# Kernel optimization log

Measured on AMD Instinct MI355X. Metric: run time of the kernel, lower is better.

Reference implementation:

```python
import jax, jax.numpy as jnp
import numpy as np

B, D, O = 128, 1024, 512
EPS = 1e-5

def setup_inputs() -> dict:
    key = jax.random.key(0)
    ks = jax.random.split(key, 12)
    s = 0.02  # truncated-normal-ish scale
    glorot1 = float(np.sqrt(6.0 / (D + O)))
    glorot3 = float(np.sqrt(6.0 / (3 * O + O)))
    return {
        "x": jax.random.normal(ks[0], (B, D), jnp.float32),
        "gt": jax.random.normal(ks[1], (D, O), jnp.float32) * s,
        "wt": jax.random.normal(ks[2], (D, O), jnp.float32) * s,
        "mt": jax.random.normal(ks[3], (D, O), jnp.float32) * s,
        "kernel_1": jax.random.uniform(ks[4], (D, O), jnp.float32, -glorot1, glorot1),
        "bias_1": jnp.zeros((O,), jnp.float32),
        "kernel_3": jax.random.uniform(ks[5], (3 * O, O), jnp.float32, -glorot3, glorot3),
        "bias_3": jnp.zeros((O,), jnp.float32),
        "emb_kernel": jax.random.normal(ks[6], (1, 1, 3 * O), jnp.float32) * s,  # conv1d kernel [1, in=1, 3O]
        "emb_bias": jnp.zeros((3 * O,), jnp.float32),
        "embeding_k": jax.random.normal(ks[7], (1, D, 1), jnp.float32) * s,
        "norm_g": jnp.ones((O,), jnp.float32),
        "norm_b": jnp.zeros((O,), jnp.float32),
    }

def reference(x, gt, wt, mt, kernel_1, bias_1, kernel_3, bias_3,
              emb_kernel, emb_bias, embeding_k, norm_g, norm_b):
    # perceptron cell (identity activation)
    c1 = x @ kernel_1 + bias_1                                  # [B,O]
    # NALU cell
    wa = jnp.tanh(wt) * jax.nn.sigmoid(mt)                      # [D,O]
    g = jax.nn.sigmoid(x @ gt)                                  # [B,O]
    a = x @ wa                                                  # [B,O]
    m = jnp.sinh(jnp.arcsinh(x) @ wa)                           # [B,O]
    c3 = g * a + (1.0 - g) * m                                  # [B,O]
    # test cell: per-feature self-attention
    e = x[..., None] * emb_kernel.reshape(1, 1, -1) + emb_bias  # [B,D,3O]
    q, k, v = jnp.split(e, 3, axis=-1)                          # each [B,D,O]
    scale = jax.lax.rsqrt(jnp.asarray(v.shape[-1], x.dtype))
    w = jnp.einsum('bdo,beo->bde', q, k) * scale                # [B,D,D]
    w = jax.nn.softmax(w, axis=-1)
    att = jnp.einsum('bde,beo->bdo', w, v)                      # [B,D,O]
    s = jnp.sum(att * embeding_k, axis=1)                       # [B,O]
    u = jnp.mean(s, axis=-1, keepdims=True)
    var = jnp.mean(jnp.square(s - u), axis=-1, keepdims=True)
    c4 = (s - u) * jax.lax.rsqrt(var + EPS) * norm_g + norm_b   # [B,O]
    feat = jnp.concatenate([c1, c3, c4], axis=-1)               # [B,3O]
    return feat @ kernel_3 + bias_3                             # [B,O]
```

## Files before the change

### kernel.cpp

```cpp
#include <hip/hip_runtime.h>
#include <hip/hip_bf16.h>
#include <math.h>

typedef unsigned short u16;
typedef unsigned int u32;
typedef __attribute__((ext_vector_type(8))) short bf16x8;
typedef __attribute__((ext_vector_type(4))) float f32x4;

#define NB 128
#define ND 1024
#define NO 512
#define EPSV 1e-5f
#define SCALEQK 0.04419417382415922f
#define LOG2E 1.4426950408889634f

static __device__ __forceinline__ float fast_exp2(float v) {
#if __has_builtin(__builtin_amdgcn_exp2f)
  return __builtin_amdgcn_exp2f(v);
#else
  return exp2f(v);
#endif
}
static __device__ __forceinline__ float fast_rcp(float v) {
#if __has_builtin(__builtin_amdgcn_rcpf)
  return __builtin_amdgcn_rcpf(v);
#else
  return 1.f / v;
#endif
}
static __device__ __forceinline__ u16 bf16_rtn(float f) {
  unsigned u = __float_as_uint(f);
  return (u16)((u + 0x7FFFu + ((u >> 16) & 1u)) >> 16);
}
static __device__ __forceinline__ float asinh_fast(float x) {
  const float ax = fabsf(x);
  const float s = sqrtf(fmaf(ax, ax, 1.f));
  return copysignf(__logf(ax + s), x);
}
static __device__ __forceinline__ float tanh_fast(float x) {
  return 1.f - 2.f * fast_rcp(fast_exp2(x * (2.f * LOG2E)) + 1.f);
}
static __device__ __forceinline__ float sig_fast(float x) {
  return fast_rcp(1.f + fast_exp2(-x * LOG2E));
}
static __device__ __forceinline__ float sinh_fast(float x) {
  const float z = fast_exp2(x * LOG2E);
  return 0.5f * (z - fast_rcp(z));
}

template <int AMODE, int WMODE>
static __device__ __forceinline__ void gemmA_tile(
    const float* __restrict__ Xf, const float* __restrict__ W0,
    const float* __restrict__ W1, float* __restrict__ outp,
    int o0, int k0, char* smem) {
  u16* Ash = (u16*)smem;
  u16* Bsh = (u16*)(smem + 32768);
  const int t = threadIdx.x;
  const int lane = t & 63;
  const int wr = (t >> 6) & 3;
  const int wc = t >> 8;

  const int rsub = t >> 4, c8 = (t & 15) * 8;
  float4 va[4], vb[4];
#pragma unroll
  for (int pass = 0; pass < 4; ++pass) {
    const size_t rowoff = (size_t)(pass * 32 + rsub) * ND + k0 + c8;
    va[pass] = *(const float4*)(Xf + rowoff);
    vb[pass] = *(const float4*)(Xf + rowoff + 4);
  }
  const int gkr = t >> 4, og = t & 15;
  const int go = o0 + og * 4;
  float4 w[4], mw[4];
#pragma unroll
  for (int kk = 0; kk < 4; ++kk) {
    w[kk] = *(const float4*)&W0[(size_t)(k0 + gkr * 4 + kk) * NO + go];
    if (WMODE) mw[kk] = *(const float4*)&W1[(size_t)(k0 + gkr * 4 + kk) * NO + go];
  }

#pragma unroll
  for (int pass = 0; pass < 4; ++pass) {
    const int row = pass * 32 + rsub;
    float e[8] = {va[pass].x, va[pass].y, va[pass].z, va[pass].w,
                  vb[pass].x, vb[pass].y, vb[pass].z, vb[pass].w};
    if (AMODE == 2) {
#pragma unroll
      for (int i = 0; i < 8; ++i) e[i] = asinh_fast(e[i]);
    }
    u16 h[8];
#pragma unroll
    for (int i = 0; i < 8; ++i) h[i] = bf16_rtn(e[i]);
    const int byte = (row * 256 + c8 * 2) ^ ((row & 7) << 4);
    *(uint4*)((char*)Ash + byte) = make_uint4(
        (u32)h[0] | ((u32)h[1] << 16), (u32)h[2] | ((u32)h[3] << 16),
        (u32)h[4] | ((u32)h[5] << 16), (u32)h[6] | ((u32)h[7] << 16));
  }
  {
    if (WMODE) {
#pragma unroll
      for (int kk = 0; kk < 4; ++kk) {
        w[kk].x = tanh_fast(w[kk].x) * sig_fast(mw[kk].x);
        w[kk].y = tanh_fast(w[kk].y) * sig_fast(mw[kk].y);
        w[kk].z = tanh_fast(w[kk].z) * sig_fast(mw[kk].z);
        w[kk].w = tanh_fast(w[kk].w) * sig_fast(mw[kk].w);
      }
    }
    const float* wp0 = (const float*)&w[0];
    const float* wp1 = (const float*)&w[1];
    const float* wp2 = (const float*)&w[2];
    const float* wp3 = (const float*)&w[3];
#pragma unroll
    for (int j = 0; j < 4; ++j) {
      const u16 h0 = bf16_rtn(wp0[j]), h1 = bf16_rtn(wp1[j]);
      const u16 h2 = bf16_rtn(wp2[j]), h3 = bf16_rtn(wp3[j]);
      const int col = og * 4 + j;
      const int byte = (col * 256 + gkr * 8) ^ ((col & 7) << 4);
      *(uint2*)((char*)Bsh + byte) =
          make_uint2((u32)h0 | ((u32)h1 << 16), (u32)h2 | ((u32)h3 << 16));
    }
  }
  __syncthreads();
  const f32x4 vz = {0.f, 0.f, 0.f, 0.f};
  f32x4 acc[2][2];
  acc[0][0] = vz; acc[0][1] = vz; acc[1][0] = vz; acc[1][1] = vz;
#pragma unroll
  for (int ks2 = 0; ks2 < 4; ++ks2) {
    const int kbyte = ks2 * 64 + (lane >> 4) * 16;
    bf16x8 a[2], b[2];
#pragma unroll
    for (int m = 0; m < 2; ++m) {
      const int row = wr * 32 + m * 16 + (lane & 15);
      a[m] = *(const bf16x8*)((const char*)Ash + ((row * 256 + kbyte) ^ ((row & 7) << 4)));
    }
#pragma unroll
    for (int n = 0; n < 2; ++n) {
      const int col = wc * 32 + n * 16 + (lane & 15);
      b[n] = *(const bf16x8*)((const char*)Bsh + ((col * 256 + kbyte) ^ ((col & 7) << 4)));
    }
#pragma unroll
    for (int m = 0; m < 2; ++m)
#pragma unroll
      for (int n = 0; n < 2; ++n)
        acc[m][n] = __builtin_amdgcn_mfma_f32_16x16x32_bf16(a[m], b[n], acc[m][n], 0, 0, 0);
  }
#pragma unroll
  for (int m = 0; m < 2; ++m)
#pragma unroll
    for (int n = 0; n < 2; ++n) {
      const int col = o0 + wc * 32 + n * 16 + (lane & 15);
#pragma unroll
      for (int r = 0; r < 4; ++r) {
        const int row = wr * 32 + m * 16 + (lane >> 4) * 4 + r;
        outp[(size_t)row * NO + col] = acc[m][n][r];
      }
    }
}

__global__ __launch_bounds__(512) void k1_fused(
    const float* __restrict__ x, const float* __restrict__ gt,
    const float* __restrict__ wt, const float* __restrict__ mt,
    const float* __restrict__ k1w, const float* __restrict__ embk,
    const float* __restrict__ embb, const float* __restrict__ ekd,
    const float* __restrict__ k3w, const float* __restrict__ ng,
    const float* __restrict__ nbv, float* __restrict__ Tfull,
    float* __restrict__ pA, float* __restrict__ U, float* __restrict__ V,
    float* __restrict__ Wc) {
  __shared__ __align__(16) char smem[49152];
  const int bid = blockIdx.x;
  const int t = threadIdx.x;
  const int wv = t >> 6;

  if (bid < NB) {
    float* xsh = (float*)smem;
    float(*red)[8] = (float(*)[8])(smem + 4096);
    float* bc = (float*)(smem + 4096 + 7 * 8 * 4);
    *(float2*)&xsh[t * 2] = *(const float2*)&x[bid * ND + t * 2];
    float s1, s3;
    {
      const float kk = embk[NO + t];
      s1 = embk[t] * kk;
      s3 = kk * embb[t];
    }
#pragma unroll
    for (int off = 32; off; off >>= 1) {
      s1 += __shfl_xor(s1, off);
      s3 += __shfl_xor(s3, off);
    }
    if ((t & 63) == 0) { red[0][wv] = s1; red[1][wv] = s3; }
    __syncthreads();
    if (t < 2) {
      float v = 0.f;
#pragma unroll
      for (int i = 0; i < 8; ++i) v += red[t][i];
      bc[t] = v;
    }
    __syncthreads();
    const float S1 = bc[0], S3 = bc[1];
    const float aL2 = SCALEQK * LOG2E * S3;
    const float dS1 = SCALEQK * S1;
    float mm[7];
#pragma unroll
    for (int k = 0; k < 7; ++k) mm[k] = 0.f;
#pragma unroll
    for (int j = 0; j < 2; ++j) {
      const float xe = xsh[t * 2 + j];
      float p = fast_exp2(aL2 * xe);
      mm[0] += p;
#pragma unroll
      for (int k = 1; k < 7; ++k) { p *= xe; mm[k] += p; }
    }
#pragma unroll
    for (int off = 32; off; off >>= 1)
#pragma unroll
      for (int k = 0; k < 7; ++k) mm[k] += __shfl_xor(mm[k], off);
    if ((t & 63) == 0)
#pragma unroll
      for (int k = 0; k < 7; ++k) red[k][wv] = mm[k];
    __syncthreads();
    if (t < 7) {
      float v = 0.f;
#pragma unroll
      for (int i = 0; i < 8; ++i) v += red[t][i];
      bc[2 + t] = v;
    }
    __syncthreads();
    const float invf[6] = {1.f, 1.f, 0.5f, 1.6666667e-1f, 4.1666668e-2f, 8.3333333e-3f};
    float cn[6], cd[6];
#pragma unroll
    for (int k = 0; k < 6; ++k) {
      cn[k] = bc[3 + k] * invf[k];
      cd[k] = bc[2 + k] * invf[k];
    }
    float Ta = 0.f;
#pragma unroll
    for (int j = 0; j < 2; ++j) {
      const int d = t * 2 + j;
      const float del = dS1 * xsh[d];
      float num = cn[5], den = cd[5];
#pragma unroll
      for (int k = 4; k >= 0; --k) {
        num = fmaf(num, del, cn[k]);
        den = fmaf(den, del, cd[k]);
      }
      Ta = fmaf(ekd[d], num / den, Ta);
    }
#pragma unroll
    for (int off = 32; off; off >>= 1) Ta += __shfl_xor(Ta, off);
    __syncthreads();
    if ((t & 63) == 0) red[0][wv] = Ta;
    __syncthreads();
    if (t == 0) {
      float v = 0.f;
#pragma unroll
      for (int i = 0; i < 8; ++i) v += red[0][i];
      Tfull[bid] = v;
    }
    return;
  }
  if (bid < 384) {
    const int b2 = bid - NB;
    const int g = b2 >> 6, ks = (b2 >> 3) & 7, ot = b2 & 7;
    float* outp = pA + (size_t)(g * 8 + ks) * (NB * NO);
    if (g == 0)
      gemmA_tile<1, 0>(x, k1w, k1w, outp, ot * 64, ks * 128, smem);
    else if (g == 1)
      gemmA_tile<1, 0>(x, gt, gt, outp, ot * 64, ks * 128, smem);
    else if (g == 2)
      gemmA_tile<1, 1>(x, wt, mt, outp, ot * 64, ks * 128, smem);
    else
      gemmA_tile<2, 1>(x, wt, mt, outp, ot * 64, ks * 128, smem);
    return;
  }
  {
    float(*lds)[64][3] = (float(*)[64][3])smem;
    __shared__ float mred[2][8];
    __shared__ float mbc[2];
    float svk = embk[2 * NO + t], svb = embb[2 * NO + t];
#pragma unroll
    for (int off = 32; off; off >>= 1) {
      svk += __shfl_xor(svk, off);
      svb += __shfl_xor(svb, off);
    }
    if ((t & 63) == 0) { mred[0][wv] = svk; mred[1][wv] = svb; }
    __syncthreads();
    if (t < 2) {
      float s = 0.f;
#pragma unroll
      for (int i = 0; i < 8; ++i) s += mred[t][i];
      mbc[t] = s * (1.f / (float)NO);
    }
    __syncthreads();
    const float mvk = mbc[0], mvb = mbc[1];
    const int jbase = (bid - 384) * 64;
    const int j = jbase + (t & 63);
    const int oc = t >> 6;
    float au = 0.f, av = 0.f, aw = 0.f;
#pragma unroll 4
    for (int oo = 0; oo < 64; ++oo) {
      const int o = oc * 64 + oo;
      const float kj = k3w[(size_t)(2 * NO + o) * NO + j];
      const float g = ng[o];
      au = fmaf((embk[2 * NO + o] - mvk) * g, kj, au);
      av = fmaf((embb[2 * NO + o] - mvb) * g, kj, av);
      aw = fmaf(nbv[o], kj, aw);
    }
    lds[oc][t & 63][0] = au;
    lds[oc][t & 63][1] = av;
    lds[oc][t & 63][2] = aw;
    __syncthreads();
    if (t < 64) {
      float su = 0.f, sv = 0.f, sw = 0.f;
#pragma unroll
      for (int cch = 0; cch < 8; ++cch) {
        su += lds[cch][t][0];
        sv += lds[cch][t][1];
        sw += lds[cch][t][2];
      }
      U[jbase + t] = su;
      V[jbase + t] = sv;
      Wc[jbase + t] = sw;
    }
  }
}

__global__ __launch_bounds__(512) void k2_combineA(
    const float* __restrict__ pA, const float* __restrict__ b1,
    const float* __restrict__ embk, const float* __restrict__ embb,
    const float* __restrict__ ekd, const float* __restrict__ Tfull,
    const float* __restrict__ U, const float* __restrict__ V,
    const float* __restrict__ Wc, const float* __restrict__ b3,
    u16* __restrict__ featB, float* __restrict__ out) {
  __shared__ float red6[6][8];
  __shared__ float bc6[6];
  const int b = blockIdx.x, t = threadIdx.x;
  const int wv = t >> 6;
  {
    const float vk = embk[2 * NO + t], vb = embb[2 * NO + t];
    float svk = vk, svb = vb, svk2 = vk * vk, svkvb = vk * vb, svb2 = vb * vb;
    float se = ekd[t] + ekd[t + 512];
#pragma unroll
    for (int off = 32; off; off >>= 1) {
      svk += __shfl_xor(svk, off); svb += __shfl_xor(svb, off);
      svk2 += __shfl_xor(svk2, off); svkvb += __shfl_xor(svkvb, off);
      svb2 += __shfl_xor(svb2, off); se += __shfl_xor(se, off);
    }
    if ((t & 63) == 0) {
      red6[0][wv] = svk; red6[1][wv] = svb; red6[2][wv] = svk2;
      red6[3][wv] = svkvb; red6[4][wv] = svb2; red6[5][wv] = se;
    }
    __syncthreads();
    if (t < 6) {
      float s = 0.f;
#pragma unroll
      for (int i = 0; i < 8; ++i) s += red6[t][i];
      bc6[t] = s;
    }
    __syncthreads();
  }
  const float inv_o = 1.f / (float)NO;
  const float mvk = bc6[0] * inv_o, mvb = bc6[1] * inv_o;
  const float Mvk2 = bc6[2] * inv_o - mvk * mvk;
  const float Mvkvb = bc6[3] * inv_o - mvk * mvb;
  const float Mvb2 = bc6[4] * inv_o - mvb * mvb;
  const float E = bc6[5];
  const float T = Tfull[b];
  const float var = T * T * Mvk2 + 2.f * T * E * Mvkvb + E * E * Mvb2;
  const float rs = rsqrtf(var + EPSV);
  const float aS = T * rs, cS = E * rs;

  const size_t off = (size_t)b * NO + t;
  float v1[8], v2[8], v3[8], v4[8];
#pragma unroll
  for (int s = 0; s < 8; ++s) {
    v1[s] = pA[(size_t)(0 * 8 + s) * (NB * NO) + off];
    v2[s] = pA[(size_t)(1 * 8 + s) * (NB * NO) + off];
    v3[s] = pA[(size_t)(2 * 8 + s) * (NB * NO) + off];
    v4[s] = pA[(size_t)(3 * 8 + s) * (NB * NO) + off];
  }
  float d1 = 0.f, d2 = 0.f, d3 = 0.f, d4 = 0.f;
#pragma unroll
  for (int s = 0; s < 8; ++s) { d1 += v1[s]; d2 += v2[s]; d3 += v3[s]; d4 += v4[s]; }
  const float c1v = d1 + b1[t];
  const float gg = sig_fast(d2);
  const float sh = sinh_fast(d4);
  const float c3v = fmaf(gg, d3 - sh, sh);
  featB[(size_t)b * ND + t] = bf16_rtn(c1v);
  featB[(size_t)b * ND + NO + t] = bf16_rtn(c3v);
  out[off] = fmaf(aS, U[t], fmaf(cS, V[t], b3[t] + Wc[t]));
}

__global__ __launch_bounds__(512) void k3_gemmB(
    const u16* __restrict__ featB, const float* __restrict__ k3w,
    float* __restrict__ out) {
  __shared__ __align__(16) char smem[32768];
  u16* Ash = (u16*)smem;
  u16* Bsh = (u16*)(smem + 16384);
  const int t = threadIdx.x;
  const int lane = t & 63;
  const int wr = (t >> 6) & 3;
  const int wc = t >> 8;
  const int rh = blockIdx.x >> 6, ks = (blockIdx.x >> 3) & 7, ot = blockIdx.x & 7;
  const int r0 = rh * 64, k0 = ks * 128, o0 = ot * 64;

  uint4 av[2];
#pragma unroll
  for (int p2 = 0; p2 < 2; ++p2) {
    const int s = t + p2 * 512;
    const int row = s >> 4, j8 = (s & 15) * 8;
    av[p2] = *(const uint4*)(featB + (size_t)(r0 + row) * ND + k0 + j8);
  }
  const int gkr = t >> 4, og = t & 15;
  const int go = o0 + og * 4;
  float4 w[4];
#pragma unroll
  for (int kk = 0; kk < 4; ++kk)
    w[kk] = *(const float4*)&k3w[(size_t)(k0 + gkr * 4 + kk) * NO + go];

#pragma unroll
  for (int p2 = 0; p2 < 2; ++p2) {
    const int s = t + p2 * 512;
    const int row = s >> 4, j8 = (s & 15) * 8;
    const int byte = (row * 256 + j8 * 2) ^ ((row & 7) << 4);
    *(uint4*)((char*)Ash + byte) = av[p2];
  }
  {
    const float* wp0 = (const float*)&w[0];
    const float* wp1 = (const float*)&w[1];
    const float* wp2 = (const float*)&w[2];
    const float* wp3 = (const float*)&w[3];
#pragma unroll
    for (int j = 0; j < 4; ++j) {
      const u16 h0 = bf16_rtn(wp0[j]), h1 = bf16_rtn(wp1[j]);
      const u16 h2 = bf16_rtn(wp2[j]), h3 = bf16_rtn(wp3[j]);
      const int col = og * 4 + j;
      const int byte = (col * 256 + gkr * 8) ^ ((col & 7) << 4);
      *(uint2*)((char*)Bsh + byte) =
          make_uint2((u32)h0 | ((u32)h1 << 16), (u32)h2 | ((u32)h3 << 16));
    }
  }
  __syncthreads();
  const f32x4 vz = {0.f, 0.f, 0.f, 0.f};
  f32x4 acc[2];
  acc[0] = vz; acc[1] = vz;
#pragma unroll
  for (int ks2 = 0; ks2 < 4; ++ks2) {
    const int kbyte = ks2 * 64 + (lane >> 4) * 16;
    const int row = wr * 16 + (lane & 15);
    const bf16x8 a = *(const bf16x8*)((const char*)Ash + ((row * 256 + kbyte) ^ ((row & 7) << 4)));
#pragma unroll
    for (int n = 0; n < 2; ++n) {
      const int col = wc * 32 + n * 16 + (lane & 15);
      const bf16x8 b = *(const bf16x8*)((const char*)Bsh + ((col * 256 + kbyte) ^ ((col & 7) << 4)));
      acc[n] = __builtin_amdgcn_mfma_f32_16x16x32_bf16(a, b, acc[n], 0, 0, 0);
    }
  }
#pragma unroll
  for (int n = 0; n < 2; ++n) {
    const int col = o0 + wc * 32 + n * 16 + (lane & 15);
#pragma unroll
    for (int r = 0; r < 4; ++r) {
      const int row = r0 + wr * 16 + (lane >> 4) * 4 + r;
      atomicAdd(&out[(size_t)row * NO + col], acc[n][r]);
    }
  }
}

extern "C" void kernel_launch(void* const* d_in, const int* in_sizes, int n_in,
                              void* d_out, int out_size, void* d_ws, size_t ws_size,
                              hipStream_t stream) {
  const float* x    = (const float*)d_in[0];
  const float* gt   = (const float*)d_in[1];
  const float* wt   = (const float*)d_in[2];
  const float* mt   = (const float*)d_in[3];
  const float* k1   = (const float*)d_in[4];
  const float* b1   = (const float*)d_in[5];
  const float* k3   = (const float*)d_in[6];
  const float* b3   = (const float*)d_in[7];
  const float* embk = (const float*)d_in[8];
  const float* embb = (const float*)d_in[9];
  const float* ekd  = (const float*)d_in[10];
  const float* ng   = (const float*)d_in[11];
  const float* nb   = (const float*)d_in[12];

  char* wsb = (char*)d_ws;
  float* Tfull = (float*)wsb;
  float* U  = (float*)(wsb + 4096);
  float* V  = (float*)(wsb + 8192);
  float* Wc = (float*)(wsb + 12288);
  float* pA = (float*)(wsb + (1u << 20));
  u16* featB = (u16*)(wsb + (10u << 20));
  float* out = (float*)d_out;

  hipLaunchKernelGGL(k1_fused, dim3(392), dim3(512), 0, stream,
                     x, gt, wt, mt, k1, embk, embb, ekd, k3, ng, nb,
                     Tfull, pA, U, V, Wc);
  hipLaunchKernelGGL(k2_combineA, dim3(128), dim3(512), 0, stream,
                     pA, b1, embk, embb, ekd, Tfull, U, V, Wc, b3, featB, out);
  hipLaunchKernelGGL(k3_gemmB, dim3(128), dim3(512), 0, stream,
                     featB, k3, out);
}
```

Baseline: 24.61 us.

## Widen GEMM-A tiles to 128 output columns to halve block count

Each GEMM-A block now covers 128 output columns instead of 64, so each wave computes a 2x4 grid of MFMA tiles rather than 2x2. The number of GEMM blocks in the fused first kernel drops from 256 to 128, and the total grid shrinks from 392 to 264. This reuses each staged x tile across twice as many columns, cutting the redundant x loads and asinh conversions. In exchange, shared memory grows to 64KB, register use per thread rises, and fewer blocks may leave some compute units idle on a chip with many CUs.

```diff
diff --git a/kernel.cpp b/kernel.cpp
--- a/kernel.cpp
+++ b/kernel.cpp
@@ -69,12 +69,15 @@
     vb[pass] = *(const float4*)(Xf + rowoff + 4);
   }
   const int gkr = t >> 4, og = t & 15;
-  const int go = o0 + og * 4;
-  float4 w[4], mw[4];
-#pragma unroll
-  for (int kk = 0; kk < 4; ++kk) {
-    w[kk] = *(const float4*)&W0[(size_t)(k0 + gkr * 4 + kk) * NO + go];
-    if (WMODE) mw[kk] = *(const float4*)&W1[(size_t)(k0 + gkr * 4 + kk) * NO + go];
+  float4 w[2][4], mw[2][4];
+#pragma unroll
+  for (int grp = 0; grp < 2; ++grp) {
+    const int go = o0 + (og + grp * 16) * 4;
+#pragma unroll
+    for (int kk = 0; kk < 4; ++kk) {
+      w[grp][kk] = *(const float4*)&W0[(size_t)(k0 + gkr * 4 + kk) * NO + go];
+      if (WMODE) mw[grp][kk] = *(const float4*)&W1[(size_t)(k0 + gkr * 4 + kk) * NO + go];
+    }
   }
 
 #pragma unroll
@@ -94,25 +97,26 @@
         (u32)h[0] | ((u32)h[1] << 16), (u32)h[2] | ((u32)h[3] << 16),
         (u32)h[4] | ((u32)h[5] << 16), (u32)h[6] | ((u32)h[7] << 16));
   }
-  {
+#pragma unroll
+  for (int grp = 0; grp < 2; ++grp) {
     if (WMODE) {
 #pragma unroll
       for (int kk = 0; kk < 4; ++kk) {
-        w[kk].x = tanh_fast(w[kk].x) * sig_fast(mw[kk].x);
-        w[kk].y = tanh_fast(w[kk].y) * sig_fast(mw[kk].y);
-        w[kk].z = tanh_fast(w[kk].z) * sig_fast(mw[kk].z);
-        w[kk].w = tanh_fast(w[kk].w) * sig_fast(mw[kk].w);
+        w[grp][kk].x = tanh_fast(w[grp][kk].x) * sig_fast(mw[grp][kk].x);
+        w[grp][kk].y = tanh_fast(w[grp][kk].y) * sig_fast(mw[grp][kk].y);
+        w[grp][kk].z = tanh_fast(w[grp][kk].z) * sig_fast(mw[grp][kk].z);
+        w[grp][kk].w = tanh_fast(w[grp][kk].w) * sig_fast(mw[grp][kk].w);
       }
     }
-    const float* wp0 = (const float*)&w[0];
-    const float* wp1 = (const float*)&w[1];
-    const float* wp2 = (const float*)&w[2];
-    const float* wp3 = (const float*)&w[3];
+    const float* wp0 = (const float*)&w[grp][0];
+    const float* wp1 = (const float*)&w[grp][1];
+    const float* wp2 = (const float*)&w[grp][2];
+    const float* wp3 = (const float*)&w[grp][3];
 #pragma unroll
     for (int j = 0; j < 4; ++j) {
       const u16 h0 = bf16_rtn(wp0[j]), h1 = bf16_rtn(wp1[j]);
       const u16 h2 = bf16_rtn(wp2[j]), h3 = bf16_rtn(wp3[j]);
-      const int col = og * 4 + j;
+      const int col = (og + grp * 16) * 4 + j;
       const int byte = (col * 256 + gkr * 8) ^ ((col & 7) << 4);
       *(uint2*)((char*)Bsh + byte) =
           make_uint2((u32)h0 | ((u32)h1 << 16), (u32)h2 | ((u32)h3 << 16));
@@ -120,33 +124,36 @@
   }
   __syncthreads();
   const f32x4 vz = {0.f, 0.f, 0.f, 0.f};
-  f32x4 acc[2][2];
-  acc[0][0] = vz; acc[0][1] = vz; acc[1][0] = vz; acc[1][1] = vz;
+  f32x4 acc[2][4];
+#pragma unroll
+  for (int m = 0; m < 2; ++m)
+#pragma unroll
+    for (int n = 0; n < 4; ++n) acc[m][n] = vz;
 #pragma unroll
   for (int ks2 = 0; ks2 < 4; ++ks2) {
     const int kbyte = ks2 * 64 + (lane >> 4) * 16;
-    bf16x8 a[2], b[2];
+    bf16x8 a[2], b[4];
 #pragma unroll
     for (int m = 0; m < 2; ++m) {
       const int row = wr * 32 + m * 16 + (lane & 15);
       a[m] = *(const bf16x8*)((const char*)Ash + ((row * 256 + kbyte) ^ ((row & 7) << 4)));
     }
 #pragma unroll
-    for (int n = 0; n < 2; ++n) {
-      const int col = wc * 32 + n * 16 + (lane & 15);
+    for (int n = 0; n < 4; ++n) {
+      const int col = wc * 64 + n * 16 + (lane & 15);
       b[n] = *(const bf16x8*)((const char*)Bsh + ((col * 256 + kbyte) ^ ((col & 7) << 4)));
     }
 #pragma unroll
     for (int m = 0; m < 2; ++m)
 #pragma unroll
-      for (int n = 0; n < 2; ++n)
+      for (int n = 0; n < 4; ++n)
         acc[m][n] = __builtin_amdgcn_mfma_f32_16x16x32_bf16(a[m], b[n], acc[m][n], 0, 0, 0);
   }
 #pragma unroll
   for (int m = 0; m < 2; ++m)
 #pragma unroll
-    for (int n = 0; n < 2; ++n) {
-      const int col = o0 + wc * 32 + n * 16 + (lane & 15);
+    for (int n = 0; n < 4; ++n) {
+      const int col = o0 + wc * 64 + n * 16 + (lane & 15);
 #pragma unroll
       for (int r = 0; r < 4; ++r) {
         const int row = wr * 32 + m * 16 + (lane >> 4) * 4 + r;
@@ -164,7 +171,7 @@
     const float* __restrict__ nbv, float* __restrict__ Tfull,
     float* __restrict__ pA, float* __restrict__ U, float* __restrict__ V,
     float* __restrict__ Wc) {
-  __shared__ __align__(16) char smem[49152];
+  __shared__ __align__(16) char smem[65536];
   const int bid = blockIdx.x;
   const int t = threadIdx.x;
   const int wv = t >> 6;
@@ -256,18 +263,19 @@
     }
     return;
   }
-  if (bid < 384) {
+  if (bid < 256) {
     const int b2 = bid - NB;
-    const int g = b2 >> 6, ks = (b2 >> 3) & 7, ot = b2 & 7;
+    const int g = b2 >> 5;
+    const int ks = (b2 >> 2) & 7, ot = b2 & 3;
     float* outp = pA + (size_t)(g * 8 + ks) * (NB * NO);
     if (g == 0)
-      gemmA_tile<1, 0>(x, k1w, k1w, outp, ot * 64, ks * 128, smem);
+      gemmA_tile<1, 0>(x, k1w, k1w, outp, ot * 128, ks * 128, smem);
     else if (g == 1)
-      gemmA_tile<1, 0>(x, gt, gt, outp, ot * 64, ks * 128, smem);
+      gemmA_tile<1, 0>(x, gt, gt, outp, ot * 128, ks * 128, smem);
     else if (g == 2)
-      gemmA_tile<1, 1>(x, wt, mt, outp, ot * 64, ks * 128, smem);
+      gemmA_tile<1, 1>(x, wt, mt, outp, ot * 128, ks * 128, smem);
     else
-      gemmA_tile<2, 1>(x, wt, mt, outp, ot * 64, ks * 128, smem);
+      gemmA_tile<2, 1>(x, wt, mt, outp, ot * 128, ks * 128, smem);
     return;
   }
   {
@@ -290,7 +298,7 @@
     }
     __syncthreads();
     const float mvk = mbc[0], mvb = mbc[1];
-    const int jbase = (bid - 384) * 64;
+    const int jbase = (bid - 256) * 64;
     const int j = jbase + (t & 63);
     const int oc = t >> 6;
     float au = 0.f, av = 0.f, aw = 0.f;
@@ -490,7 +498,7 @@
   u16* featB = (u16*)(wsb + (10u << 20));
   float* out = (float*)d_out;
 
-  hipLaunchKernelGGL(k1_fused, dim3(392), dim3(512), 0, stream,
+  hipLaunchKernelGGL(k1_fused, dim3(264), dim3(512), 0, stream,
                      x, gt, wt, mt, k1, embk, embb, ekd, k3, ng, nb,
                      Tfull, pA, U, V, Wc);
   hipLaunchKernelGGL(k2_combineA, dim3(128), dim3(512), 0, stream,
```

New measurement: 25.33 us. 2.9% more time.
